# Kernel optimization log

Hardware: AMD Instinct MI355X
Metric: run time of the kernel (lower is better)

The kernel has to match this reference:

```python
import jax, jax.numpy as jnp
import numpy as np

BN_EPS = 1e-3


def _knn_group(p1, p2, k):
    # p1, p2: [N, 3]. For each point in p1 find k nearest in p2.
    d2 = (jnp.sum(p1 * p1, -1)[:, None] + jnp.sum(p2 * p2, -1)[None, :]
          - 2.0 * (p1 @ p2.T))                      # [N, N]
    _, idx = jax.lax.top_k(-d2, k)                   # [N, k]
    nn = p2[idx]                                     # [N, k, 3]
    resi = nn - p1[:, None, :]                       # [N, k, 3]
    dist = jnp.linalg.norm(resi, axis=-1, keepdims=True)
    feat = jnp.concatenate([resi, dist], axis=-1)    # [N, k, 4]
    return feat, nn


def _conv_bn_relu(x, W, b, g, be):
    # x: [B, Cin, N, K]; 1x1 conv == channel matmul, BN uses batch stats (train mode)
    y = jnp.einsum('oi,binK->bonK', W, x) + b[None, :, None, None]
    m = jnp.mean(y, axis=(0, 2, 3), keepdims=True)
    v = jnp.var(y, axis=(0, 2, 3), keepdims=True)
    y = g[None, :, None, None] * (y - m) * jax.lax.rsqrt(v + BN_EPS) + be[None, :, None, None]
    return jax.nn.relu(y)


def setup_inputs() -> dict:
    key = jax.random.key(0)
    ks = jax.random.split(key, 8)
    B, N, k = 4, 4096, 32
    C = [4, 64, 64, 128]
    inp = {
        'points1': jax.random.normal(ks[0], (B, 3, N), jnp.float32),
        'points2': jax.random.normal(ks[1], (B, 3, N), jnp.float32),
        'k': k,
        't': jax.random.uniform(ks[2], (B,), jnp.float32),
    }
    for i in range(3):
        kw = jax.random.fold_in(ks[3], i)
        inp[f'W{i+1}'] = jax.random.normal(kw, (C[i + 1], C[i]), jnp.float32) * (1.0 / np.sqrt(C[i]))
        inp[f'b{i+1}'] = jnp.zeros((C[i + 1],), jnp.float32)
        inp[f'g{i+1}'] = jnp.ones((C[i + 1],), jnp.float32)
        inp[f'be{i+1}'] = jnp.zeros((C[i + 1],), jnp.float32)
    return inp


def reference(points1, points2, k, t, W1, b1, g1, be1, W2, b2, g2, be2, W3, b3, g3, be3):
    p1 = jnp.transpose(points1, (0, 2, 1))           # [B, N, 3]
    p2 = jnp.transpose(points2, (0, 2, 1))
    knn = jax.vmap(_knn_group, in_axes=(0, 0, None))
    f1, nn1 = knn(p1, p1, k)                          # [B, N, k, 4], [B, N, k, 3]
    f2, nn2 = knn(p1, p2, k)
    feats = jnp.concatenate([f1, f2], axis=2)         # [B, N, 2k, 4]
    grouped = jnp.concatenate([nn1, nn2], axis=2)     # [B, N, 2k, 3]
    x = jnp.transpose(feats, (0, 3, 1, 2))            # [B, 4, N, 2k]
    x = _conv_bn_relu(x, W1, b1, g1, be1)
    x = _conv_bn_relu(x, W2, b2, g2, be2)
    x = _conv_bn_relu(x, W3, b3, g3, be3)             # [B, 128, N, 2k]
    scores = jnp.max(x, axis=1)                       # [B, N, 2k]
    w = jax.nn.softmax(scores, axis=-1)               # [B, N, 2k]
    fused = jnp.einsum('bnk,bnkc->bcn', w, grouped)   # [B, 3, N]
    return fused
```

## Files before the change

kernel.cpp:

```cpp
#include <hip/hip_runtime.h>
#include <hip/hip_bf16.h>

#define B_   4
#define N_   4096
#define KNN_ 32
#define KK_  64
#define MTOT 1048576
#define BN_EPS 1e-3f

typedef unsigned int u32;
typedef unsigned long long u64;
typedef __attribute__((ext_vector_type(8))) short bf16x8;
typedef __attribute__((ext_vector_type(4))) float f32x4;

__device__ __forceinline__ ushort f2bf_bits(float f) {
    u32 b = __float_as_uint(f);
    b += 0x7fffu + ((b >> 16) & 1u);
    return (ushort)(b >> 16);
}

__global__ __launch_bounds__(256, 3) void knn_kernel(
    const float* __restrict__ p1, const float* __restrict__ p2,
    float* __restrict__ feats, float* __restrict__ mom)
{
    __shared__ float2 cxy[N_];
    __shared__ float  cz[N_];
    __shared__ float  part[4][14];

    const int tid  = threadIdx.x;
    const int wave = tid >> 6, lane = tid & 63;
    const int pb    = blockIdx.x / 96;
    const int chunk = blockIdx.x % 96;
    const int pr = pb >> 2, b = pb & 3;
    const int start = (chunk * 4096) / 96;
    const int end   = ((chunk + 1) * 4096) / 96;

    const float* srcb = (pr ? p2 : p1) + (size_t)b * 3 * N_;
    for (int n = tid; n < N_; n += 256) {
        float x = srcb[n], y = srcb[N_ + n], z = srcb[2*N_ + n];
        cxy[n] = make_float2(x, y);
        cz[n]  = z;
    }
    __syncthreads();

    const float* p1b = p1 + (size_t)b * 3 * N_;
    const u64 below = (1ull << lane) - 1ull;

    float mm[14];
    #pragma unroll
    for (int s = 0; s < 14; ++s) mm[s] = 0.f;

    for (int n = start + wave; n < end; n += 4) {
        float qx, qy, qz;
        if (pr == 0) { float2 q = cxy[n]; qx = q.x; qy = q.y; qz = cz[n]; }
        else         { qx = p1b[n]; qy = p1b[N_ + n]; qz = p1b[2*N_ + n]; }
        const float s1 = fmaf(qx, qx, fmaf(qy, qy, qz*qz));

        u32 keys[64];
        u32 a0 = 0xFFFFFFFFu, a1 = 0xFFFFFFFFu, a2 = 0xFFFFFFFFu, a3 = 0xFFFFFFFFu;
        u32 b0 = 0xFFFFFFFFu, b1 = 0xFFFFFFFFu, b2 = 0xFFFFFFFFu, b3 = 0xFFFFFFFFu;
        #pragma unroll
        for (int j = 0; j < 32; ++j) {
            {
                float2 cA = cxy[j * 64 + lane];
                float  zA = cz[j * 64 + lane];
                float cw  = fmaf(cA.x, cA.x, fmaf(cA.y, cA.y, zA*zA));
                float dot = fmaf(qx, cA.x, fmaf(qy, cA.y, qz * zA));
                float d2  = fmaf(-2.0f, dot, s1 + cw);
                u32 u = __float_as_uint(d2);
                u32 key = u ^ (u32)(((int)u >> 31) | 0x80000000);
                keys[j] = key;
                a3 = min(a3, key);
                u32 t;
                t = min(a2, a3); a3 = max(a2, a3); a2 = t;
                t = min(a1, a2); a2 = max(a1, a2); a1 = t;
                t = min(a0, a1); a1 = max(a0, a1); a0 = t;
            }
            {
                float2 cB = cxy[(j + 32) * 64 + lane];
                float  zB = cz[(j + 32) * 64 + lane];
                float cw  = fmaf(cB.x, cB.x, fmaf(cB.y, cB.y, zB*zB));
                float dot = fmaf(qx, cB.x, fmaf(qy, cB.y, qz * zB));
                float d2  = fmaf(-2.0f, dot, s1 + cw);
                u32 u = __float_as_uint(d2);
                u32 key = u ^ (u32)(((int)u >> 31) | 0x80000000);
                keys[j + 32] = key;
                b3 = min(b3, key);
                u32 t;
                t = min(b2, b3); b3 = max(b2, b3); b2 = t;
                t = min(b1, b2); b2 = max(b1, b2); b1 = t;
                t = min(b0, b1); b1 = max(b0, b1); b0 = t;
            }
        }
        u32 k0 = a0, k1 = a1, k2 = a2, k3 = a3;
        #pragma unroll
        for (int m = 0; m < 4; ++m) {
            u32 x = (m == 0) ? b0 : (m == 1) ? b1 : (m == 2) ? b2 : b3;
            k3 = min(k3, x);
            u32 t;
            t = min(k2, k3); k3 = max(k2, k3); k2 = t;
            t = min(k1, k2); k2 = max(k1, k2); k1 = t;
            t = min(k0, k1); k1 = max(k0, k1); k0 = t;
        }

        u32 mn = k0, mx = k3;
        #pragma unroll
        for (int off = 1; off < 64; off <<= 1) {
            mn = min(mn, (u32)__shfl_xor((int)mn, off, 64));
            mx = max(mx, (u32)__shfl_xor((int)mx, off, 64));
        }
        u32 lo = mn, hi = mx;
        while (lo < hi) {
            u32 mid = lo + ((hi - lo) >> 1);
            int c = __popcll(__ballot(k0 <= mid)) + __popcll(__ballot(k1 <= mid))
                  + __popcll(__ballot(k2 <= mid)) + __popcll(__ballot(k3 <= mid));
            if (c >= 32) hi = mid; else lo = mid + 1;
        }
        u32 T = lo;

        int nl;
        if (__ballot(k3 <= T) == 0ull) {
            nl = __popcll(__ballot(k0 < T)) + __popcll(__ballot(k1 < T))
               + __popcll(__ballot(k2 < T)) + __popcll(__ballot(k3 < T));
        } else {
            nl = 0;
            #pragma unroll
            for (int j = 0; j < 64; ++j) nl += __popcll(__ballot(keys[j] < T));
            if (nl > 31) {
                lo = 0u; hi = T;
                while (lo < hi) {
                    u32 mid = lo + ((hi - lo) >> 1);
                    int c = 0;
                    #pragma unroll
                    for (int j = 0; j < 64; ++j) c += __popcll(__ballot(keys[j] <= mid));
                    if (c >= 32) hi = mid; else lo = mid + 1;
                }
                T = lo;
                nl = 0;
                #pragma unroll
                for (int j = 0; j < 64; ++j) nl += __popcll(__ballot(keys[j] < T));
            }
        }
        const int need_eq = 32 - nl;

        float* fout = feats + ((size_t)(b * N_ + n) * KK_ + pr * KNN_) * 4;
        int base = 0, eq_seen = 0;
        #pragma unroll
        for (int j = 0; j < 64; ++j) {
            u32 key = keys[j];
            bool lt = key < T;
            bool eq = key == T;
            u64 mlt = __ballot(lt);
            u64 meq = __ballot(eq);
            if (mlt | meq) {
                int slot = -1;
                if (lt) slot = base + __popcll(mlt & below);
                else if (eq) {
                    int es = eq_seen + __popcll(meq & below);
                    if (es < need_eq) slot = nl + es;
                }
                if (slot >= 0) {
                    float2 cx2 = cxy[j * 64 + lane];
                    float  cz1 = cz[j * 64 + lane];
                    float rx = cx2.x - qx, ry = cx2.y - qy, rz = cz1 - qz;
                    float dist = sqrtf(fmaf(rx, rx, fmaf(ry, ry, rz*rz)));
                    *(float4*)(fout + slot * 4) = make_float4(rx, ry, rz, dist);
                    mm[0] += rx; mm[1] += ry; mm[2] += rz; mm[3] += dist;
                    mm[4]  = fmaf(rx, rx, mm[4]);   mm[5]  = fmaf(rx, ry, mm[5]);
                    mm[6]  = fmaf(rx, rz, mm[6]);   mm[7]  = fmaf(rx, dist, mm[7]);
                    mm[8]  = fmaf(ry, ry, mm[8]);   mm[9]  = fmaf(ry, rz, mm[9]);
                    mm[10] = fmaf(ry, dist, mm[10]); mm[11] = fmaf(rz, rz, mm[11]);
                    mm[12] = fmaf(rz, dist, mm[12]); mm[13] = fmaf(dist, dist, mm[13]);
                }
                base    += __popcll(mlt);
                eq_seen += __popcll(meq);
            }
        }
    }

    #pragma unroll
    for (int s = 0; s < 14; ++s) {
        #pragma unroll
        for (int off = 1; off < 64; off <<= 1) mm[s] += __shfl_xor(mm[s], off, 64);
    }
    if (lane == 0) {
        #pragma unroll
        for (int s = 0; s < 14; ++s) part[wave][s] = mm[s];
    }
    __syncthreads();
    if (tid < 14) {
        float v = part[0][tid] + part[1][tid] + part[2][tid] + part[3][tid];
        atomicAdd(&mom[tid * 16], v);
    }
}

__global__ __launch_bounds__(256) void conv2_mfma(
    const float* __restrict__ feats,
    const float* __restrict__ W1,
    const float* __restrict__ g1, const float* __restrict__ be1,
    const float* __restrict__ W2,
    const float* __restrict__ mom,
    ushort* __restrict__ y2F, float* __restrict__ s2S, float* __restrict__ s2Q)
{
    __shared__ float statS[64], statQ[64];
    const int tid = threadIdx.x;
    const int wid = tid >> 6, l = tid & 63, q = l >> 4, i = l & 15;
    if (tid < 64) { statS[tid] = 0.f; statQ[tid] = 0.f; }

    const float invM = 1.0f / MTOT;
    const float M0 = mom[0*16], M1 = mom[1*16], M2 = mom[2*16], M3 = mom[3*16];
    const float Sxx = mom[4*16],  Sxy = mom[5*16],  Sxz = mom[6*16],  Sxd = mom[7*16];
    const float Syy = mom[8*16],  Syz = mom[9*16],  Syd = mom[10*16];
    const float Szz = mom[11*16], Szd = mom[12*16], Sdd = mom[13*16];

    float4 w1f[16];
    float  c1v[16];
    #pragma unroll
    for (int h = 0; h < 2; ++h)
      #pragma unroll
      for (int j = 0; j < 8; ++j) {
        int ci = h*32 + q*8 + j;
        float w0 = W1[ci*4+0], w1 = W1[ci*4+1], w2 = W1[ci*4+2], w3 = W1[ci*4+3];
        float meanf = (w0*M0 + w1*M1 + w2*M2 + w3*M3) * invM;
        float qq = w0*(w0*Sxx + 2.f*(w1*Sxy + w2*Sxz + w3*Sxd))
                 + w1*(w1*Syy + 2.f*(w2*Syz + w3*Syd))
                 + w2*(w2*Szz + 2.f*w3*Szd)
                 + w3*w3*Sdd;
        float var = qq * invM - meanf * meanf;
        float sc  = g1[ci] * rsqrtf(var + BN_EPS);
        w1f[h*8+j] = make_float4(sc*w0, sc*w1, sc*w2, sc*w3);
        c1v[h*8+j] = fmaf(-sc, meanf, be1[ci]);
      }
    bf16x8 a2[4][2];
    #pragma unroll
    for (int t = 0; t < 4; ++t)
      #pragma unroll
      for (int h = 0; h < 2; ++h)
        #pragma unroll
        for (int j = 0; j < 8; ++j)
          a2[t][h][j] = (short)f2bf_bits(W2[(t*16 + i)*64 + h*32 + q*8 + j]);

    float ssum[16], ssq[16];
    #pragma unroll
    for (int s = 0; s < 16; ++s) { ssum[s] = 0.f; ssq[s] = 0.f; }
    __syncthreads();

    for (int r16 = 0; r16 < 16; ++r16) {
        const int row = blockIdx.x * 16 + r16;
        float4 f = ((const float4*)feats)[row*64 + wid*16 + i];
        bf16x8 xb[2];
        #pragma unroll
        for (int h = 0; h < 2; ++h)
          #pragma unroll
          for (int j = 0; j < 8; ++j) {
            float4 w = w1f[h*8+j];
            float x = fmaxf(fmaf(w.x, f.x, fmaf(w.y, f.y, fmaf(w.z, f.z, fmaf(w.w, f.w, c1v[h*8+j])))), 0.f);
            xb[h][j] = (short)f2bf_bits(x);
          }
        f32x4 acc[4];
        #pragma unroll
        for (int t = 0; t < 4; ++t) acc[t] = (f32x4){0.f,0.f,0.f,0.f};
        #pragma unroll
        for (int t = 0; t < 4; ++t) {
            acc[t] = __builtin_amdgcn_mfma_f32_16x16x32_bf16(a2[t][0], xb[0], acc[t], 0, 0, 0);
            acc[t] = __builtin_amdgcn_mfma_f32_16x16x32_bf16(a2[t][1], xb[1], acc[t], 0, 0, 0);
        }
        ushort* wp = y2F + row*4096 + wid*1024 + q*64 + i*4;
        #pragma unroll
        for (int t = 0; t < 4; ++t) {
            #pragma unroll
            for (int reg = 0; reg < 4; ++reg) {
                float y = acc[t][reg];
                ssum[t*4+reg] += y;
                ssq[t*4+reg]  = fmaf(y, y, ssq[t*4+reg]);
            }
            uint2 pk;
            pk.x = (u32)f2bf_bits(acc[t][0]) | ((u32)f2bf_bits(acc[t][1]) << 16);
            pk.y = (u32)f2bf_bits(acc[t][2]) | ((u32)f2bf_bits(acc[t][3]) << 16);
            *(uint2*)(wp + t*256) = pk;
        }
    }
    #pragma unroll
    for (int s = 0; s < 16; ++s) {
        #pragma unroll
        for (int off = 1; off < 16; off <<= 1) {
            ssum[s] += __shfl_xor(ssum[s], off, 64);
            ssq[s]  += __shfl_xor(ssq[s],  off, 64);
        }
    }
    if (i == 0) {
        #pragma unroll
        for (int s = 0; s < 16; ++s) {
            int co = (s >> 2)*16 + q*4 + (s & 3);
            atomicAdd(&statS[co], ssum[s]);
            atomicAdd(&statQ[co], ssq[s]);
        }
    }
    __syncthreads();
    if (tid < 64) { atomicAdd(&s2S[tid], statS[tid]); atomicAdd(&s2Q[tid], statQ[tid]); }
}

__global__ __launch_bounds__(256) void conv3_stats(
    ushort* __restrict__ y2F,
    const float* __restrict__ g2, const float* __restrict__ be2,
    const float* __restrict__ W3,
    const float* __restrict__ s2S, const float* __restrict__ s2Q,
    float* __restrict__ s3S, float* __restrict__ s3Q)
{
    __shared__ float statS[128], statQ[128];
    const int tid = threadIdx.x;
    const int w = tid >> 6, l = tid & 63, q = l >> 4, i = l & 15;
    const int ph = w >> 1, oh = w & 1;
    if (tid < 128) { statS[tid] = 0.f; statQ[tid] = 0.f; }

    float sc2v[16], sh2v[16];
    #pragma unroll
    for (int h = 0; h < 2; ++h)
      #pragma unroll
      for (int j = 0; j < 8; ++j) {
        int ci = h*32 + q*8 + j;
        float m  = s2S[ci] * (1.0f / MTOT);
        float v  = s2Q[ci] * (1.0f / MTOT) - m * m;
        float sc = g2[ci] * rsqrtf(v + BN_EPS);
        sc2v[h*8+j] = sc;
        sh2v[h*8+j] = fmaf(-sc, m, be2[ci]);
      }
    bf16x8 a3[4][2];
    #pragma unroll
    for (int t = 0; t < 4; ++t)
      #pragma unroll
      for (int h = 0; h < 2; ++h)
        #pragma unroll
        for (int j = 0; j < 8; ++j)
          a3[t][h][j] = (short)f2bf_bits(W3[((oh*4 + t)*16 + i)*64 + h*32 + q*8 + j]);

    float ssum[16], ssq[16];
    #pragma unroll
    for (int s = 0; s < 16; ++s) { ssum[s] = 0.f; ssq[s] = 0.f; }

    for (int r16 = 0; r16 < 16; ++r16) {
        const int row = blockIdx.x * 16 + r16;
        ushort* rp0 = y2F + row*4096 + (2*ph)*1024 + q*128 + i*4;
        ushort* rp1 = rp0 + 1024;
        uint2 a00 = *(const uint2*)(rp0);       uint2 a01 = *(const uint2*)(rp0 + 64);
        uint2 a10 = *(const uint2*)(rp0 + 512); uint2 a11 = *(const uint2*)(rp0 + 576);
        uint2 b00 = *(const uint2*)(rp1);       uint2 b01 = *(const uint2*)(rp1 + 64);
        uint2 b10 = *(const uint2*)(rp1 + 512); uint2 b11 = *(const uint2*)(rp1 + 576);

        bf16x8 xa[2], xc[2];
        #pragma unroll
        for (int pt2 = 0; pt2 < 2; ++pt2) {
            uint2 v00 = pt2 ? b00 : a00, v01 = pt2 ? b01 : a01;
            uint2 v10 = pt2 ? b10 : a10, v11 = pt2 ? b11 : a11;
            bf16x8* dst = pt2 ? xc : xa;
            #pragma unroll
            for (int h = 0; h < 2; ++h) {
                u32 w0 = h ? v10.x : v00.x, w1 = h ? v10.y : v00.y;
                u32 w2 = h ? v11.x : v01.x, w3 = h ? v11.y : v01.y;
                float xf[8];
                xf[0] = __uint_as_float(w0 << 16); xf[1] = __uint_as_float(w0 & 0xffff0000u);
                xf[2] = __uint_as_float(w1 << 16); xf[3] = __uint_as_float(w1 & 0xffff0000u);
                xf[4] = __uint_as_float(w2 << 16); xf[5] = __uint_as_float(w2 & 0xffff0000u);
                xf[6] = __uint_as_float(w3 << 16); xf[7] = __uint_as_float(w3 & 0xffff0000u);
                #pragma unroll
                for (int j = 0; j < 8; ++j) {
                    float x = fmaxf(fmaf(sc2v[h*8+j], xf[j], sh2v[h*8+j]), 0.f);
                    dst[h][j] = (short)f2bf_bits(x);
                }
            }
        }
        __syncthreads();
        if (oh == 0) {
            uint4 ua0 = *(uint4*)&xa[0], ua1 = *(uint4*)&xa[1];
            uint4 uc0 = *(uint4*)&xc[0], uc1 = *(uint4*)&xc[1];
            *(uint2*)(rp0)       = make_uint2(ua0.x, ua0.y);
            *(uint2*)(rp0 + 64)  = make_uint2(ua0.z, ua0.w);
            *(uint2*)(rp0 + 512) = make_uint2(ua1.x, ua1.y);
            *(uint2*)(rp0 + 576) = make_uint2(ua1.z, ua1.w);
            *(uint2*)(rp1)       = make_uint2(uc0.x, uc0.y);
            *(uint2*)(rp1 + 64)  = make_uint2(uc0.z, uc0.w);
            *(uint2*)(rp1 + 512) = make_uint2(uc1.x, uc1.y);
            *(uint2*)(rp1 + 576) = make_uint2(uc1.z, uc1.w);
        }
        #pragma unroll
        for (int t = 0; t < 4; ++t) {
            f32x4 A = (f32x4){0.f,0.f,0.f,0.f};
            A = __builtin_amdgcn_mfma_f32_16x16x32_bf16(a3[t][0], xa[0], A, 0, 0, 0);
            A = __builtin_amdgcn_mfma_f32_16x16x32_bf16(a3[t][1], xa[1], A, 0, 0, 0);
            f32x4 Bv = (f32x4){0.f,0.f,0.f,0.f};
            Bv = __builtin_amdgcn_mfma_f32_16x16x32_bf16(a3[t][0], xc[0], Bv, 0, 0, 0);
            Bv = __builtin_amdgcn_mfma_f32_16x16x32_bf16(a3[t][1], xc[1], Bv, 0, 0, 0);
            #pragma unroll
            for (int reg = 0; reg < 4; ++reg) {
                float ya = A[reg], yb = Bv[reg];
                ssum[t*4+reg] += ya + yb;
                ssq[t*4+reg]  = fmaf(ya, ya, fmaf(yb, yb, ssq[t*4+reg]));
            }
        }
    }
    #pragma unroll
    for (int s = 0; s < 16; ++s) {
        #pragma unroll
        for (int off = 1; off < 16; off <<= 1) {
            ssum[s] += __shfl_xor(ssum[s], off, 64);
            ssq[s]  += __shfl_xor(ssq[s],  off, 64);
        }
    }
    if (i == 0) {
        #pragma unroll
        for (int s = 0; s < 16; ++s) {
            int co = oh*64 + (s >> 2)*16 + q*4 + (s & 3);
            atomicAdd(&statS[co], ssum[s]);
            atomicAdd(&statQ[co], ssq[s]);
        }
    }
    __syncthreads();
    if (tid < 128) { atomicAdd(&s3S[tid], statS[tid]); atomicAdd(&s3Q[tid], statQ[tid]); }
}

__global__ __launch_bounds__(256) void conv3_final(
    const ushort* __restrict__ x3F,
    const float* __restrict__ W3,
    const float* __restrict__ g3, const float* __restrict__ be3,
    const float* __restrict__ s3S, const float* __restrict__ s3Q,
    const float4* __restrict__ feats4, const float* __restrict__ p1,
    float* __restrict__ outp)
{
    __shared__ float sc3L[128], sh3L[128];
    __shared__ float s2L[2][2][64];
    const int tid = threadIdx.x;
    const int w = tid >> 6, l = tid & 63, q = l >> 4, i = l & 15;
    const int ph = w >> 1, oh = w & 1;

    if (tid < 128) {
        float m  = s3S[tid] * (1.0f / MTOT);
        float v  = s3Q[tid] * (1.0f / MTOT) - m * m;
        float sc = g3[tid] * rsqrtf(v + BN_EPS);
        sc3L[tid] = sc;
        sh3L[tid] = fmaf(-sc, m, be3[tid]);
    }
    bf16x8 a3[4][2];
    #pragma unroll
    for (int t = 0; t < 4; ++t)
      #pragma unroll
      for (int h = 0; h < 2; ++h)
        #pragma unroll
        for (int j = 0; j < 8; ++j)
          a3[t][h][j] = (short)f2bf_bits(W3[((oh*4 + t)*16 + i)*64 + h*32 + q*8 + j]);
    __syncthreads();

    for (int r16 = 0; r16 < 16; ++r16) {
        const int row = blockIdx.x * 16 + r16;
        #pragma unroll
        for (int pt2 = 0; pt2 < 2; ++pt2) {
            const int pt = 2*ph + pt2;
            const ushort* rp = x3F + row*4096 + pt*1024 + q*128 + i*4;
            uint2 u00 = *(const uint2*)(rp);       uint2 u01 = *(const uint2*)(rp + 64);
            uint2 u10 = *(const uint2*)(rp + 512); uint2 u11 = *(const uint2*)(rp + 576);
            uint4 v0 = make_uint4(u00.x, u00.y, u01.x, u01.y);
            uint4 v1 = make_uint4(u10.x, u10.y, u11.x, u11.y);
            bf16x8 xb0 = *(bf16x8*)&v0, xb1 = *(bf16x8*)&v1;
            float mx = -3.4e38f;
            #pragma unroll
            for (int t = 0; t < 4; ++t) {
                f32x4 a = (f32x4){0.f,0.f,0.f,0.f};
                a = __builtin_amdgcn_mfma_f32_16x16x32_bf16(a3[t][0], xb0, a, 0, 0, 0);
                a = __builtin_amdgcn_mfma_f32_16x16x32_bf16(a3[t][1], xb1, a, 0, 0, 0);
                const int co = oh*64 + t*16 + q*4;
                float4 s4 = *(const float4*)&sc3L[co];
                float4 h4 = *(const float4*)&sh3L[co];
                mx = fmaxf(mx, fmaf(s4.x, a[0], h4.x));
                mx = fmaxf(mx, fmaf(s4.y, a[1], h4.y));
                mx = fmaxf(mx, fmaf(s4.z, a[2], h4.z));
                mx = fmaxf(mx, fmaf(s4.w, a[3], h4.w));
            }
            mx = fmaxf(mx, __shfl_xor(mx, 16, 64));
            mx = fmaxf(mx, __shfl_xor(mx, 32, 64));
            if (q == 0) s2L[r16 & 1][oh][pt*16 + i] = mx;
        }
        __syncthreads();
        if (w == 0) {
            float sc = fmaxf(fmaxf(s2L[r16 & 1][0][l], s2L[r16 & 1][1][l]), 0.f);
            float m2 = sc;
            #pragma unroll
            for (int off = 1; off < 64; off <<= 1) m2 = fmaxf(m2, __shfl_xor(m2, off, 64));
            float e = __expf(sc - m2);
            float se = e;
            #pragma unroll
            for (int off = 1; off < 64; off <<= 1) se += __shfl_xor(se, off, 64);
            float wgt = e / se;
            const int bb = row >> 12, n = row & 4095;
            float qx = p1[(size_t)bb*3*N_ + n];
            float qy = p1[(size_t)bb*3*N_ + N_ + n];
            float qz = p1[(size_t)bb*3*N_ + 2*N_ + n];
            float4 f4 = feats4[row*64 + l];
            float ox = wgt * (f4.x + qx), oy = wgt * (f4.y + qy), oz = wgt * (f4.z + qz);
            #pragma unroll
            for (int off = 1; off < 64; off <<= 1) {
                ox += __shfl_xor(ox, off, 64);
                oy += __shfl_xor(oy, off, 64);
                oz += __shfl_xor(oz, off, 64);
            }
            if (l == 0) {
                outp[bb*3*N_ + 0*N_ + n] = ox;
                outp[bb*3*N_ + 1*N_ + n] = oy;
                outp[bb*3*N_ + 2*N_ + n] = oz;
            }
        }
    }
}

extern "C" void kernel_launch(void* const* d_in, const int* in_sizes, int n_in,
                              void* d_out, int out_size, void* d_ws, size_t ws_size,
                              hipStream_t stream)
{
    const float* p1  = (const float*)d_in[0];
    const float* p2  = (const float*)d_in[1];
    const float* W1  = (const float*)d_in[4];
    const float* g1  = (const float*)d_in[6];
    const float* be1 = (const float*)d_in[7];
    const float* W2  = (const float*)d_in[8];
    const float* g2  = (const float*)d_in[10];
    const float* be2 = (const float*)d_in[11];
    const float* W3  = (const float*)d_in[12];
    const float* g3  = (const float*)d_in[14];
    const float* be3 = (const float*)d_in[15];

    char* ws = (char*)d_ws;
    const size_t OFF_FEATS = 4096;
    const size_t OFF_Y2    = OFF_FEATS + (size_t)MTOT * 4 * 4;
    const size_t NEEDED    = OFF_Y2 + (size_t)MTOT * 64 * 2;
    if (ws_size < NEEDED) return;

    float* s2S = (float*)(ws + 512);  float* s2Q = (float*)(ws + 768);
    float* s3S = (float*)(ws + 1024); float* s3Q = (float*)(ws + 1536);
    float* mom = (float*)(ws + 2048);
    float* feats = (float*)(ws + OFF_FEATS);
    ushort* y2F  = (ushort*)(ws + OFF_Y2);

    hipMemsetAsync(ws, 0, 4096, stream);

    knn_kernel<<<768, 256, 0, stream>>>(p1, p2, feats, mom);
    conv2_mfma<<<1024, 256, 0, stream>>>(feats, W1, g1, be1, W2, mom,
                                         y2F, s2S, s2Q);
    conv3_stats<<<1024, 256, 0, stream>>>(y2F, g2, be2, W3,
                                          s2S, s2Q, s3S, s3Q);
    conv3_final<<<1024, 256, 0, stream>>>(y2F, W3, g3, be3, s3S, s3Q,
                                          (const float4*)feats, p1,
                                          (float*)d_out);
}
```

Measured before the change: 479.1 us.

## Recompute distances instead of caching keys, use fmed3 top-4, double block size

The kNN kernel drops the 64-entry per-lane key array and recomputes candidate distances from LDS in the threshold and emit passes. This cuts register pressure so blocks of 512 threads with higher occupancy fit. The top-4 insertion now uses float fmed3 instead of integer min/max swaps. The ranking metric also drops the constant query-norm term. The cost is redoing the distance arithmetic and LDS reads in later passes, and slightly different floating-point rounding for ties.

```diff
diff --git a/kernel.cpp b/kernel.cpp
--- a/kernel.cpp
+++ b/kernel.cpp
@@ -19,13 +19,33 @@
     return (ushort)(b >> 16);
 }
 
-__global__ __launch_bounds__(256, 3) void knn_kernel(
+__device__ __forceinline__ float med3f(float a, float b, float c) {
+    return __builtin_amdgcn_fmed3f(a, b, c);
+}
+
+__device__ __forceinline__ float rank_e(float cx, float cy, float cz_,
+                                        float qx, float qy, float qz) {
+    float cw  = fmaf(cx, cx, fmaf(cy, cy, cz_ * cz_));
+    float dot = fmaf(qx, cx, fmaf(qy, cy, qz * cz_));
+    return fmaf(-2.0f, dot, cw);
+}
+
+__device__ __forceinline__ u32 ordkey(float f) {
+    u32 u = __float_as_uint(f);
+    return u ^ (u32)(((int)u >> 31) | 0x80000000);
+}
+__device__ __forceinline__ float ordinv(u32 k) {
+    u32 u = (k & 0x80000000u) ? (k ^ 0x80000000u) : ~k;
+    return __uint_as_float(u);
+}
+
+__global__ __launch_bounds__(512, 6) void knn_kernel(
     const float* __restrict__ p1, const float* __restrict__ p2,
     float* __restrict__ feats, float* __restrict__ mom)
 {
     __shared__ float2 cxy[N_];
     __shared__ float  cz[N_];
-    __shared__ float  part[4][14];
+    __shared__ float  part[8][14];
 
     const int tid  = threadIdx.x;
     const int wave = tid >> 6, lane = tid & 63;
@@ -36,7 +56,7 @@
     const int end   = ((chunk + 1) * 4096) / 96;
 
     const float* srcb = (pr ? p2 : p1) + (size_t)b * 3 * N_;
-    for (int n = tid; n < N_; n += 256) {
+    for (int n = tid; n < N_; n += 512) {
         float x = srcb[n], y = srcb[N_ + n], z = srcb[2*N_ + n];
         cxy[n] = make_float2(x, y);
         cz[n]  = z;
@@ -45,63 +65,49 @@
 
     const float* p1b = p1 + (size_t)b * 3 * N_;
     const u64 below = (1ull << lane) - 1ull;
+    const float FMAX = 3.402823466e+38f;
 
     float mm[14];
     #pragma unroll
     for (int s = 0; s < 14; ++s) mm[s] = 0.f;
 
-    for (int n = start + wave; n < end; n += 4) {
+    for (int n = start + wave; n < end; n += 8) {
         float qx, qy, qz;
         if (pr == 0) { float2 q = cxy[n]; qx = q.x; qy = q.y; qz = cz[n]; }
         else         { qx = p1b[n]; qy = p1b[N_ + n]; qz = p1b[2*N_ + n]; }
-        const float s1 = fmaf(qx, qx, fmaf(qy, qy, qz*qz));
-
-        u32 keys[64];
-        u32 a0 = 0xFFFFFFFFu, a1 = 0xFFFFFFFFu, a2 = 0xFFFFFFFFu, a3 = 0xFFFFFFFFu;
-        u32 b0 = 0xFFFFFFFFu, b1 = 0xFFFFFFFFu, b2 = 0xFFFFFFFFu, b3 = 0xFFFFFFFFu;
+
+        float A0 = FMAX, A1 = FMAX, A2 = FMAX, A3 = FMAX;
+        float B0 = FMAX, B1 = FMAX, B2 = FMAX, B3 = FMAX;
         #pragma unroll
         for (int j = 0; j < 32; ++j) {
             {
-                float2 cA = cxy[j * 64 + lane];
-                float  zA = cz[j * 64 + lane];
-                float cw  = fmaf(cA.x, cA.x, fmaf(cA.y, cA.y, zA*zA));
-                float dot = fmaf(qx, cA.x, fmaf(qy, cA.y, qz * zA));
-                float d2  = fmaf(-2.0f, dot, s1 + cw);
-                u32 u = __float_as_uint(d2);
-                u32 key = u ^ (u32)(((int)u >> 31) | 0x80000000);
-                keys[j] = key;
-                a3 = min(a3, key);
-                u32 t;
-                t = min(a2, a3); a3 = max(a2, a3); a2 = t;
-                t = min(a1, a2); a2 = max(a1, a2); a1 = t;
-                t = min(a0, a1); a1 = max(a0, a1); a0 = t;
+                float2 c = cxy[j * 64 + lane];
+                float  z = cz[j * 64 + lane];
+                float  e = rank_e(c.x, c.y, z, qx, qy, qz);
+                A3 = med3f(e, A2, A3);
+                A2 = med3f(e, A1, A2);
+                A1 = med3f(e, A0, A1);
+                A0 = fminf(A0, e);
             }
             {
-                float2 cB = cxy[(j + 32) * 64 + lane];
-                float  zB = cz[(j + 32) * 64 + lane];
-                float cw  = fmaf(cB.x, cB.x, fmaf(cB.y, cB.y, zB*zB));
-                float dot = fmaf(qx, cB.x, fmaf(qy, cB.y, qz * zB));
-                float d2  = fmaf(-2.0f, dot, s1 + cw);
-                u32 u = __float_as_uint(d2);
-                u32 key = u ^ (u32)(((int)u >> 31) | 0x80000000);
-                keys[j + 32] = key;
-                b3 = min(b3, key);
-                u32 t;
-                t = min(b2, b3); b3 = max(b2, b3); b2 = t;
-                t = min(b1, b2); b2 = max(b1, b2); b1 = t;
-                t = min(b0, b1); b1 = max(b0, b1); b0 = t;
-            }
-        }
-        u32 k0 = a0, k1 = a1, k2 = a2, k3 = a3;
+                float2 c = cxy[(j + 32) * 64 + lane];
+                float  z = cz[(j + 32) * 64 + lane];
+                float  e = rank_e(c.x, c.y, z, qx, qy, qz);
+                B3 = med3f(e, B2, B3);
+                B2 = med3f(e, B1, B2);
+                B1 = med3f(e, B0, B1);
+                B0 = fminf(B0, e);
+            }
+        }
         #pragma unroll
         for (int m = 0; m < 4; ++m) {
-            u32 x = (m == 0) ? b0 : (m == 1) ? b1 : (m == 2) ? b2 : b3;
-            k3 = min(k3, x);
-            u32 t;
-            t = min(k2, k3); k3 = max(k2, k3); k2 = t;
-            t = min(k1, k2); k2 = max(k1, k2); k1 = t;
-            t = min(k0, k1); k1 = max(k0, k1); k0 = t;
-        }
+            float x = (m == 0) ? B0 : (m == 1) ? B1 : (m == 2) ? B2 : B3;
+            A3 = med3f(x, A2, A3);
+            A2 = med3f(x, A1, A2);
+            A1 = med3f(x, A0, A1);
+            A0 = fminf(A0, x);
+        }
+        u32 k0 = ordkey(A0), k1 = ordkey(A1), k2 = ordkey(A2), k3 = ordkey(A3);
 
         u32 mn = k0, mx = k3;
         #pragma unroll
@@ -123,33 +129,53 @@
             nl = __popcll(__ballot(k0 < T)) + __popcll(__ballot(k1 < T))
                + __popcll(__ballot(k2 < T)) + __popcll(__ballot(k3 < T));
         } else {
+            float Tf0 = ordinv(T);
             nl = 0;
-            #pragma unroll
-            for (int j = 0; j < 64; ++j) nl += __popcll(__ballot(keys[j] < T));
+            #pragma unroll 1
+            for (int j = 0; j < 64; ++j) {
+                float2 c = cxy[(j << 6) + lane];
+                float  z = cz[(j << 6) + lane];
+                float  e = rank_e(c.x, c.y, z, qx, qy, qz);
+                nl += __popcll(__ballot(e < Tf0));
+            }
             if (nl > 31) {
-                lo = 0u; hi = T;
-                while (lo < hi) {
-                    u32 mid = lo + ((hi - lo) >> 1);
+                u32 lo2 = 0u, hi2 = T;
+                while (lo2 < hi2) {
+                    u32 mid = lo2 + ((hi2 - lo2) >> 1);
                     int c = 0;
-                    #pragma unroll
-                    for (int j = 0; j < 64; ++j) c += __popcll(__ballot(keys[j] <= mid));
-                    if (c >= 32) hi = mid; else lo = mid + 1;
+                    #pragma unroll 1
+                    for (int j = 0; j < 64; ++j) {
+                        float2 cc = cxy[(j << 6) + lane];
+                        float  z  = cz[(j << 6) + lane];
+                        float  e  = rank_e(cc.x, cc.y, z, qx, qy, qz);
+                        c += __popcll(__ballot(ordkey(e) <= mid));
+                    }
+                    if (c >= 32) hi2 = mid; else lo2 = mid + 1;
                 }
-                T = lo;
+                T = lo2;
+                float Tf1 = ordinv(T);
                 nl = 0;
-                #pragma unroll
-                for (int j = 0; j < 64; ++j) nl += __popcll(__ballot(keys[j] < T));
+                #pragma unroll 1
+                for (int j = 0; j < 64; ++j) {
+                    float2 c = cxy[(j << 6) + lane];
+                    float  z = cz[(j << 6) + lane];
+                    float  e = rank_e(c.x, c.y, z, qx, qy, qz);
+                    nl += __popcll(__ballot(e < Tf1));
+                }
             }
         }
         const int need_eq = 32 - nl;
+        const float Tf = ordinv(T);
 
         float* fout = feats + ((size_t)(b * N_ + n) * KK_ + pr * KNN_) * 4;
         int base = 0, eq_seen = 0;
         #pragma unroll
         for (int j = 0; j < 64; ++j) {
-            u32 key = keys[j];
-            bool lt = key < T;
-            bool eq = key == T;
+            float2 c = cxy[j * 64 + lane];
+            float  z = cz[j * 64 + lane];
+            float  e = rank_e(c.x, c.y, z, qx, qy, qz);
+            bool lt = e < Tf;
+            bool eq = e == Tf;
             u64 mlt = __ballot(lt);
             u64 meq = __ballot(eq);
             if (mlt | meq) {
@@ -160,9 +186,7 @@
                     if (es < need_eq) slot = nl + es;
                 }
                 if (slot >= 0) {
-                    float2 cx2 = cxy[j * 64 + lane];
-                    float  cz1 = cz[j * 64 + lane];
-                    float rx = cx2.x - qx, ry = cx2.y - qy, rz = cz1 - qz;
+                    float rx = c.x - qx, ry = c.y - qy, rz = z - qz;
                     float dist = sqrtf(fmaf(rx, rx, fmaf(ry, ry, rz*rz)));
                     *(float4*)(fout + slot * 4) = make_float4(rx, ry, rz, dist);
                     mm[0] += rx; mm[1] += ry; mm[2] += rz; mm[3] += dist;
@@ -189,7 +213,8 @@
     }
     __syncthreads();
     if (tid < 14) {
-        float v = part[0][tid] + part[1][tid] + part[2][tid] + part[3][tid];
+        float v = part[0][tid] + part[1][tid] + part[2][tid] + part[3][tid]
+                + part[4][tid] + part[5][tid] + part[6][tid] + part[7][tid];
         atomicAdd(&mom[tid * 16], v);
     }
 }
@@ -540,7 +565,7 @@
 
     hipMemsetAsync(ws, 0, 4096, stream);
 
-    knn_kernel<<<768, 256, 0, stream>>>(p1, p2, feats, mom);
+    knn_kernel<<<768, 512, 0, stream>>>(p1, p2, feats, mom);
     conv2_mfma<<<1024, 256, 0, stream>>>(feats, W1, g1, be1, W2, mom,
                                          y2F, s2S, s2Q);
     conv3_stats<<<1024, 256, 0, stream>>>(y2F, g2, be2, W3,
```

Result: slower. 692.9 us (+44.6%).
